# Kernel tuning notes

Measured on AMD Instinct MI355X. Metric: run time of the kernel, lower is better.

The kernel has to match this reference:

```python
import jax, jax.numpy as jnp
import numpy as np

N = 50000          # num nodes
E_RAND = 600000    # random edges (self-loops appended -> E = E_RAND + N)
HEADS = 4
OUT_CH = 16
OUT_NEURONS = 2 * OUT_CH   # diag reparam: [mean | std-logit]
IN_CH = 128
NEG_SLOPE = 0.2


def setup_inputs() -> dict:
    key = jax.random.key(0)
    k1, k2, k3, k4, k5 = jax.random.split(key, 5)
    x = jax.random.normal(k1, (N, IN_CH), jnp.float32)
    src = jax.random.randint(k2, (E_RAND,), 0, N, jnp.int32)
    dst = jax.random.randint(k3, (E_RAND,), 0, N, jnp.int32)
    loops = jnp.arange(N, dtype=jnp.int32)
    edge_index = jnp.stack([jnp.concatenate([src, loops]),
                            jnp.concatenate([dst, loops])])  # [2, E]
    # glorot init for weight [IN_CH, HEADS*OUT_NEURONS]
    s_w = float(np.sqrt(6.0 / (IN_CH + HEADS * OUT_NEURONS)))
    weight = jax.random.uniform(k4, (IN_CH, HEADS * OUT_NEURONS), jnp.float32, -s_w, s_w)
    # glorot for att [1, HEADS, 2*OUT_NEURONS]
    s_a = float(np.sqrt(6.0 / (HEADS + 2 * OUT_NEURONS)))
    att = jax.random.uniform(k5, (1, HEADS, 2 * OUT_NEURONS), jnp.float32, -s_a, s_a)
    bias = jnp.zeros((HEADS * OUT_NEURONS,), jnp.float32)
    return {"x": x, "edge_index": edge_index, "weight": weight, "att": att, "bias": bias}


def reference(x, edge_index, weight, att, bias):
    src, dst = edge_index[0], edge_index[1]  # j -> i (PyG source_to_target)
    h = (x @ weight).reshape(N, HEADS, OUT_NEURONS)          # Theta x
    x_j = h[src]                                             # [E, H, On]
    x_i = h[dst]                                             # [E, H, On]
    # alpha = LeakyReLU(a^T [x_i || x_j])
    alpha = (x_i * att[:, :, :OUT_NEURONS]).sum(-1) + \
            (x_j * att[:, :, OUT_NEURONS:]).sum(-1)          # [E, H]
    alpha = jax.nn.leaky_relu(alpha, NEG_SLOPE)
    # segment softmax over neighborhoods of target node i
    m = jax.ops.segment_max(alpha, dst, num_segments=N)      # [N, H]
    e = jnp.exp(alpha - m[dst])
    denom = jax.ops.segment_sum(e, dst, num_segments=N)      # [N, H]
    alpha = e / (denom[dst] + 1e-16)                          # [E, H]
    # scatter-add aggregation of attention-weighted features
    agg = jax.ops.segment_sum(x_j * alpha[:, :, None], dst, num_segments=N)  # [N, H, On]
    out = agg.reshape(N, HEADS * OUT_NEURONS) + bias
    # VIB diag reparameterization + closed-form KL against N(0, I)
    o = out.reshape(N * HEADS, OUT_NEURONS)
    mean = o[:, :OUT_CH]
    std = jax.nn.softplus(o[:, OUT_CH:] - 5.0) + 1e-10
    kl = (-jnp.log(std) + 0.5 * (std * std + mean * mean) - 0.5).sum(-1)  # [N*H]
    ixz = kl.reshape(N, HEADS).mean(-1)                      # [N]
    # eval + val_use_mean=True: output is the mean part
    out_final = mean.reshape(N, HEADS * OUT_CH)
    structure_kl_loss = jnp.zeros((), jnp.float32)
    return out_final, ixz, structure_kl_loss, mean, std
```

## Files before the change

kernel.cpp:

```cpp
#include <hip/hip_runtime.h>
#include <stdint.h>

#define NN 50000
#define NB 196
#define NTILES 782
#define NEG_SLOPE 0.2f
#define WTS 136

#define IXZ_OFF    (NN * 64)
#define SKL_OFF    (NN * 64 + NN)
#define MEAN_OFF   (NN * 64 + NN + 1)
#define STD_OFF    (MEAN_OFF + NN * 64)

typedef unsigned int u32;
typedef unsigned short u16;
typedef unsigned char u8;
typedef __attribute__((ext_vector_type(8))) short short8;
typedef __attribute__((ext_vector_type(4))) float f32x4;
typedef __attribute__((ext_vector_type(2))) float f32x2;

__device__ __forceinline__ float bf2f(u16 s) { return __uint_as_float(((u32)s) << 16); }
__device__ __forceinline__ u16 f2bf(float f) {
    u32 u = __float_as_uint(f);
    u += 0x7FFFu + ((u >> 16) & 1u);
    return (u16)(u >> 16);
}
__device__ __forceinline__ float lo16(u32 u) { return __uint_as_float(u << 16); }
__device__ __forceinline__ float hi16(u32 u) { return __uint_as_float(u & 0xFFFF0000u); }
__device__ __forceinline__ float softplusf(float x) {
    return fmaxf(x, 0.f) + log1pf(expf(-fabsf(x)));
}
__device__ __forceinline__ void stout(void* o, long long idx, float v, bool f32) {
    if (f32) ((float*)o)[idx] = v;
    else     ((u16*)o)[idx]   = f2bf(v);
}
__device__ __forceinline__ int wscan_incl(int v, int lane) {
#pragma unroll
    for (int off = 1; off < 64; off <<= 1) {
        int u = __shfl_up(v, off);
        if (lane >= off) v += u;
    }
    return v;
}

__device__ __forceinline__ bool detect_f32_block(const u32* __restrict__ xw,
                                                 int* lflag)
{
    const int t = threadIdx.x;
    if (t < 64) {
        u32 wrd = xw[t];
        u32 e = (wrd >> 7) & 0xFF;
        bool plaus = (e >= 0x60 && e <= 0x85);
        unsigned long long b = __ballot(plaus);
        if (t == 0) *lflag = (__popcll(b) < 32) ? 1 : 0;
    }
    __syncthreads();
    return *lflag != 0;
}

__global__ __launch_bounds__(256) void k_wt(const void* __restrict__ xv,
                                            const void* __restrict__ wv_,
                                            u16* __restrict__ wtg,
                                            int* __restrict__ zbase)
{
    __shared__ int lflag;
    const bool f32 = detect_f32_block((const u32*)xv, &lflag);
    const int t = threadIdx.x;

    for (int i = blockIdx.x * 256 + t; i < 2 * NN + 1; i += 64 * 256)
        zbase[i] = 0;

    if (blockIdx.x < 8) {
        const int k = blockIdx.x * 16 + (t >> 4);
        const int cq = t & 15;
        u16 v[8];
        if (f32) {
            const float* w = (const float*)wv_;
            float4 a = *(const float4*)(w + k * 128 + cq * 8);
            float4 b = *(const float4*)(w + k * 128 + cq * 8 + 4);
            v[0] = f2bf(a.x); v[1] = f2bf(a.y); v[2] = f2bf(a.z); v[3] = f2bf(a.w);
            v[4] = f2bf(b.x); v[5] = f2bf(b.y); v[6] = f2bf(b.z); v[7] = f2bf(b.w);
        } else {
            const u16* w = (const u16*)wv_;
            uint4 u = *(const uint4*)(w + k * 128 + cq * 8);
            v[0] = (u16)(u.x & 0xFFFF); v[1] = (u16)(u.x >> 16);
            v[2] = (u16)(u.y & 0xFFFF); v[3] = (u16)(u.y >> 16);
            v[4] = (u16)(u.z & 0xFFFF); v[5] = (u16)(u.z >> 16);
            v[6] = (u16)(u.w & 0xFFFF); v[7] = (u16)(u.w >> 16);
        }
#pragma unroll
        for (int j = 0; j < 8; j++)
            wtg[(cq * 8 + j) * WTS + k] = v[j];
    }
}

__global__ __launch_bounds__(256) void k_gemm(
    const void* __restrict__ xv, const u16* __restrict__ wtg,
    const void* __restrict__ attv, u8* __restrict__ hb,
    float* __restrict__ ai, float* __restrict__ aj,
    const int* __restrict__ dst, int* __restrict__ counts, int E)
{
    __shared__ __align__(16) u16 ls[128 * WTS];
    __shared__ int lflag;
    const bool f32 = detect_f32_block((const u32*)xv, &lflag);
    const int tid = threadIdx.x;

    {
        uint4* d = (uint4*)ls;
        const uint4* s = (const uint4*)wtg;
        for (int i = tid; i < 128 * WTS / 8; i += 256) d[i] = s[i];
    }

    const int w = tid >> 6, L = tid & 63;
    const int q = L >> 4, c15 = L & 15;
    const int nb16 = blockIdx.x * 64 + w * 16;

    short8 afr[4];
    {
        int nrow = nb16 + c15; if (nrow > NN - 1) nrow = NN - 1;
        if (f32) {
            const float* xp = (const float*)xv + (size_t)nrow * 128 + q * 8;
#pragma unroll
            for (int ks = 0; ks < 4; ks++) {
                float4 a = *(const float4*)(xp + ks * 32);
                float4 b = *(const float4*)(xp + ks * 32 + 4);
                union { short8 s; u16 e[8]; } u;
                u.e[0] = f2bf(a.x); u.e[1] = f2bf(a.y); u.e[2] = f2bf(a.z); u.e[3] = f2bf(a.w);
                u.e[4] = f2bf(b.x); u.e[5] = f2bf(b.y); u.e[6] = f2bf(b.z); u.e[7] = f2bf(b.w);
                afr[ks] = u.s;
            }
        } else {
            const u16* xp = (const u16*)xv + (size_t)nrow * 128 + q * 8;
#pragma unroll
            for (int ks = 0; ks < 4; ks++)
                afr[ks] = *(const short8*)(xp + ks * 32);
        }
    }
    __syncthreads();

    f32x4 acc[8];
#pragma unroll
    for (int t = 0; t < 8; t++) {
        acc[t] = (f32x4){0.f, 0.f, 0.f, 0.f};
        const u16* bp = ls + (16 * t + c15) * WTS + q * 8;
#pragma unroll
        for (int ks = 0; ks < 4; ks++) {
            short8 bfr = *(const short8*)(bp + ks * 32);
            acc[t] = __builtin_amdgcn_mfma_f32_16x16x32_bf16(afr[ks], bfr, acc[t], 0, 0, 0);
        }
    }

    float ati[8], atj[8];
#pragma unroll
    for (int t = 0; t < 8; t++) {
        int p = (t >> 1) * 64 + (t & 1) * 16 + c15;
        if (f32) {
            ati[t] = ((const float*)attv)[p];
            atj[t] = ((const float*)attv)[p + 32];
        } else {
            ati[t] = bf2f(((const u16*)attv)[p]);
            atj[t] = bf2f(((const u16*)attv)[p + 32]);
        }
    }
#pragma unroll
    for (int r = 0; r < 4; r++) {
        int node = nb16 + q * 4 + r;
#pragma unroll
        for (int h = 0; h < 4; h++) {
            float pi = acc[2 * h][r] * ati[2 * h] + acc[2 * h + 1][r] * ati[2 * h + 1];
            float pj = acc[2 * h][r] * atj[2 * h] + acc[2 * h + 1][r] * atj[2 * h + 1];
            pi += __shfl_xor(pi, 1); pj += __shfl_xor(pj, 1);
            pi += __shfl_xor(pi, 2); pj += __shfl_xor(pj, 2);
            pi += __shfl_xor(pi, 4); pj += __shfl_xor(pj, 4);
            pi += __shfl_xor(pi, 8); pj += __shfl_xor(pj, 8);
            if (c15 == 0 && node < NN) { ai[node * 4 + h] = pi; aj[node * 4 + h] = pj; }
        }
    }

    __syncthreads();
    u16* myls = ls + w * 16 * WTS;
#pragma unroll
    for (int t = 0; t < 8; t++)
#pragma unroll
        for (int r = 0; r < 4; r++)
            myls[(q * 4 + r) * WTS + 16 * t + c15] = f2bf(acc[t][r]);
#pragma unroll
    for (int v = 0; v < 4; v++) {
        int idx = v * 64 + L;
        int nrow = idx >> 4, c8 = idx & 15;
        int node = nb16 + nrow;
        uint4 t16 = *(const uint4*)(myls + nrow * WTS + c8 * 8);
        float f0 = lo16(t16.x), f1 = hi16(t16.x);
        float f2 = lo16(t16.y), f3 = hi16(t16.y);
        float f4 = lo16(t16.z), f5 = hi16(t16.z);
        float f6 = lo16(t16.w), f7 = hi16(t16.w);
        u32 lo = 0, hi = 0;
        lo = __builtin_amdgcn_cvt_pk_fp8_f32(f0, f1, lo, false);
        lo = __builtin_amdgcn_cvt_pk_fp8_f32(f2, f3, lo, true);
        hi = __builtin_amdgcn_cvt_pk_fp8_f32(f4, f5, hi, false);
        hi = __builtin_amdgcn_cvt_pk_fp8_f32(f6, f7, hi, true);
        if (node < NN) {
            uint2 o; o.x = lo; o.y = hi;
            *(uint2*)(hb + (size_t)node * 128 + c8 * 8) = o;
        }
    }

    const int gid = blockIdx.x * 256 + tid;
    const int stride = gridDim.x * 256;
    for (int e = gid; e < E; e += stride)
        atomicAdd(&counts[dst[e]], 1);
}

__global__ __launch_bounds__(256) void k_scan1(const int* __restrict__ counts,
                                               int* __restrict__ lexcl,
                                               int* __restrict__ blocksum,
                                               int* __restrict__ done,
                                               int* __restrict__ sboff_g)
{
    __shared__ int wsum[4];
    __shared__ int sboff[256];
    __shared__ int lastf;
    const int t = threadIdx.x, lane = t & 63, wv = t >> 6;
    const int i = blockIdx.x * 256 + t;
    int c = (i < NN) ? counts[i] : 0;
    int inc = wscan_incl(c, lane);
    if (lane == 63) wsum[wv] = inc;
    __syncthreads();
    int add = 0;
#pragma unroll
    for (int k = 0; k < 3; k++) if (k < wv) add += wsum[k];
    inc += add;
    if (i < NN) lexcl[i] = inc - c;
    if (t == 255) {
        blocksum[blockIdx.x] = inc;
        __threadfence();
        lastf = (atomicAdd(done, 1) == NB - 1) ? 1 : 0;
    }
    __syncthreads();
    if (lastf) {
        __threadfence();
        int c2 = (t < NB) ? blocksum[t] : 0;
        int inc2 = wscan_incl(c2, lane);
        if (lane == 63) wsum[wv] = inc2;
        __syncthreads();
        int add2 = 0;
#pragma unroll
        for (int k = 0; k < 3; k++) if (k < wv) add2 += wsum[k];
        sboff[t] = inc2 + add2 - c2;
        __syncthreads();
        sboff_g[t] = sboff[t];
    }
}

__global__ __launch_bounds__(256) void k_fill(
    const int* __restrict__ ei, const int* __restrict__ lexcl,
    const int* __restrict__ sboff_g, int* __restrict__ cursor,
    int* __restrict__ perm_src, int E)
{
    int e = blockIdx.x * 256 + threadIdx.x;
    if (e >= E) return;
    int d = ei[E + e];
    int pos = sboff_g[d >> 8] + lexcl[d] + atomicAdd(&cursor[d], 1);
    perm_src[pos] = ei[e];
}

__global__ __launch_bounds__(256) void k_agg(
    const int* __restrict__ lexcl, const int* __restrict__ sboff_g,
    const int* __restrict__ counts, const int* __restrict__ perm_src,
    const float* __restrict__ ai, const float* __restrict__ aj,
    const u8* __restrict__ hb, const void* __restrict__ biasv,
    const void* __restrict__ xv, void* __restrict__ outv)
{
    __shared__ int lflag;
    const bool f32 = detect_f32_block((const u32*)xv, &lflag);
    const int t = blockIdx.x * 256 + threadIdx.x;
    const int node = t >> 4;
    const int l = t & 15;
    const int head = l >> 2;
    const int cc0 = (l & 3) << 3;

    const int rs = sboff_g[node >> 8] + lexcl[node];
    const int re = rs + counts[node];
    const float ain = ai[node * 4 + head];
    const u8* hl8 = hb + l * 8;

    float dsum = 0.f;
    float a0 = 0.f, a1 = 0.f, a2 = 0.f, a3 = 0.f;
    float a4 = 0.f, a5 = 0.f, a6 = 0.f, a7 = 0.f;

    int i = rs;
    for (; i + 1 < re; i += 2) {
        int s0 = perm_src[i], s1 = perm_src[i + 1];
        float x0 = aj[s0 * 4 + head] + ain;
        float x1 = aj[s1 * 4 + head] + ain;
        x0 = x0 > 0.f ? x0 : NEG_SLOPE * x0;
        x1 = x1 > 0.f ? x1 : NEG_SLOPE * x1;
        float e0 = __expf(x0), e1 = __expf(x1);
        uint2 h0 = *(const uint2*)(hl8 + (size_t)s0 * 128);
        uint2 h1 = *(const uint2*)(hl8 + (size_t)s1 * 128);
        f32x2 p0 = __builtin_amdgcn_cvt_pk_f32_fp8(h0.x, false);
        f32x2 p1 = __builtin_amdgcn_cvt_pk_f32_fp8(h0.x, true);
        f32x2 p2 = __builtin_amdgcn_cvt_pk_f32_fp8(h0.y, false);
        f32x2 p3 = __builtin_amdgcn_cvt_pk_f32_fp8(h0.y, true);
        f32x2 q0 = __builtin_amdgcn_cvt_pk_f32_fp8(h1.x, false);
        f32x2 q1 = __builtin_amdgcn_cvt_pk_f32_fp8(h1.x, true);
        f32x2 q2 = __builtin_amdgcn_cvt_pk_f32_fp8(h1.y, false);
        f32x2 q3 = __builtin_amdgcn_cvt_pk_f32_fp8(h1.y, true);
        dsum += e0 + e1;
        a0 += e0 * p0.x + e1 * q0.x;  a1 += e0 * p0.y + e1 * q0.y;
        a2 += e0 * p1.x + e1 * q1.x;  a3 += e0 * p1.y + e1 * q1.y;
        a4 += e0 * p2.x + e1 * q2.x;  a5 += e0 * p2.y + e1 * q2.y;
        a6 += e0 * p3.x + e1 * q3.x;  a7 += e0 * p3.y + e1 * q3.y;
    }
    if (i < re) {
        int s0 = perm_src[i];
        float x0 = aj[s0 * 4 + head] + ain;
        x0 = x0 > 0.f ? x0 : NEG_SLOPE * x0;
        float e0 = __expf(x0);
        uint2 h0 = *(const uint2*)(hl8 + (size_t)s0 * 128);
        f32x2 p0 = __builtin_amdgcn_cvt_pk_f32_fp8(h0.x, false);
        f32x2 p1 = __builtin_amdgcn_cvt_pk_f32_fp8(h0.x, true);
        f32x2 p2 = __builtin_amdgcn_cvt_pk_f32_fp8(h0.y, false);
        f32x2 p3 = __builtin_amdgcn_cvt_pk_f32_fp8(h0.y, true);
        dsum += e0;
        a0 += e0 * p0.x; a1 += e0 * p0.y;
        a2 += e0 * p1.x; a3 += e0 * p1.y;
        a4 += e0 * p2.x; a5 += e0 * p2.y;
        a6 += e0 * p3.x; a7 += e0 * p3.y;
    }

    const float inv = 1.f / (dsum + 1e-16f);
    const int cb = head * 32 + cc0;
    float v[8];
    if (f32) {
        const float* bias = (const float*)biasv;
#pragma unroll
        for (int j = 0; j < 8; j++) v[j] = bias[cb + j];
    } else {
        const u16* bias = (const u16*)biasv;
#pragma unroll
        for (int j = 0; j < 8; j++) v[j] = bf2f(bias[cb + j]);
    }
    v[0] += a0 * inv; v[1] += a1 * inv; v[2] += a2 * inv; v[3] += a3 * inv;
    v[4] += a4 * inv; v[5] += a5 * inv; v[6] += a6 * inv; v[7] += a7 * inv;

    float part = 0.f;
    if (cc0 < 16) {
#pragma unroll
        for (int j = 0; j < 8; j++) part += 0.5f * v[j] * v[j];
        long long o = (long long)node * 64 + head * 16 + cc0;
#pragma unroll
        for (int j = 0; j < 8; j++) stout(outv, o + j, v[j], f32);
        long long om = (long long)MEAN_OFF + o;
#pragma unroll
        for (int j = 0; j < 8; j++) stout(outv, om + j, v[j], f32);
    } else {
        long long os = (long long)STD_OFF + (long long)node * 64 + head * 16 + (cc0 - 16);
#pragma unroll
        for (int j = 0; j < 8; j++) {
            float s = softplusf(v[j] - 5.f) + 1e-10f;
            part += -logf(s) + 0.5f * s * s - 0.5f;
            stout(outv, os + j, s, f32);
        }
    }
    part += __shfl_xor(part, 1); part += __shfl_xor(part, 2);
    part += __shfl_xor(part, 4); part += __shfl_xor(part, 8);
    if (l == 0) stout(outv, (long long)IXZ_OFF + node, part * 0.25f, f32);
    if (t == 0) stout(outv, (long long)SKL_OFF, 0.f, f32);
}

extern "C" void kernel_launch(void* const* d_in, const int* in_sizes, int n_in,
                              void* d_out, int out_size, void* d_ws, size_t ws_size,
                              hipStream_t stream)
{
    const void* x    = d_in[0];
    const int*  ei   = (const int*)d_in[1];
    const void* w    = d_in[2];
    const void* att  = d_in[3];
    const void* bias = d_in[4];
    int E = in_sizes[1] / 2;

    u8*    hb       = (u8*)d_ws;
    float* ai       = (float*)(hb + (size_t)NN * 128);
    float* aj       = ai + NN * 4;
    int*   perm_src = (int*)(aj + NN * 4);
    int*   counts   = perm_src + E;
    int*   cursor   = counts + NN;
    int*   done     = cursor + NN;
    int*   lexcl    = done + 1;
    int*   blocksum = lexcl + NN;
    int*   sboff_g  = blocksum + NB;
    u16*   wtg      = (u16*)(((uintptr_t)(sboff_g + 256) + 15) & ~(uintptr_t)15);

    k_wt<<<64, 256, 0, stream>>>(x, w, wtg, counts);
    k_gemm<<<NTILES, 256, 0, stream>>>(x, wtg, att, hb, ai, aj,
                                       ei + E, counts, E);
    k_scan1<<<NB, 256, 0, stream>>>(counts, lexcl, blocksum, done, sboff_g);
    k_fill<<<(E + 255) / 256, 256, 0, stream>>>(ei, lexcl, sboff_g,
                                                cursor, perm_src, E);
    k_agg<<<(NN * 16) / 256, 256, 0, stream>>>(lexcl, sboff_g, counts,
                                               perm_src, ai, aj, hb,
                                               bias, x, d_out);
}
```

Baseline: 208.2 us.

## Split edge counting into its own kernel, read GEMM weights from global, prefetch indices

The dst-count atomics move out of the GEMM into a separate k_cnt kernel. The GEMM stops staging the whole transposed weight in LDS and reads B fragments straight from global/L2, using only small per-wave LDS regions for the fp8 repack, which cuts LDS use per block and removes two barriers. The aggregation loop software-prefetches the next pair of source indices and aj logits so the gathers overlap the current iteration's work. A redundant LDS round-trip in the scan's block-offset write is also dropped. These trade an extra kernel launch and repeated global weight reads for higher occupancy and better latency hiding.

```diff
diff --git a/kernel.cpp b/kernel.cpp
--- a/kernel.cpp
+++ b/kernel.cpp
@@ -94,22 +94,22 @@
     }
 }
 
+__global__ __launch_bounds__(256) void k_cnt(const int* __restrict__ dst,
+                                             int* __restrict__ counts, int E)
+{
+    int e = blockIdx.x * 256 + threadIdx.x;
+    if (e < E) atomicAdd(&counts[dst[e]], 1);
+}
+
 __global__ __launch_bounds__(256) void k_gemm(
     const void* __restrict__ xv, const u16* __restrict__ wtg,
     const void* __restrict__ attv, u8* __restrict__ hb,
-    float* __restrict__ ai, float* __restrict__ aj,
-    const int* __restrict__ dst, int* __restrict__ counts, int E)
-{
-    __shared__ __align__(16) u16 ls[128 * WTS];
+    float* __restrict__ ai, float* __restrict__ aj)
+{
+    __shared__ __align__(16) u16 rp[4][16 * WTS];
     __shared__ int lflag;
     const bool f32 = detect_f32_block((const u32*)xv, &lflag);
     const int tid = threadIdx.x;
-
-    {
-        uint4* d = (uint4*)ls;
-        const uint4* s = (const uint4*)wtg;
-        for (int i = tid; i < 128 * WTS / 8; i += 256) d[i] = s[i];
-    }
 
     const int w = tid >> 6, L = tid & 63;
     const int q = L >> 4, c15 = L & 15;
@@ -136,13 +136,12 @@
                 afr[ks] = *(const short8*)(xp + ks * 32);
         }
     }
-    __syncthreads();
 
     f32x4 acc[8];
 #pragma unroll
     for (int t = 0; t < 8; t++) {
         acc[t] = (f32x4){0.f, 0.f, 0.f, 0.f};
-        const u16* bp = ls + (16 * t + c15) * WTS + q * 8;
+        const u16* bp = wtg + (16 * t + c15) * WTS + q * 8;
 #pragma unroll
         for (int ks = 0; ks < 4; ks++) {
             short8 bfr = *(const short8*)(bp + ks * 32);
@@ -177,8 +176,7 @@
         }
     }
 
-    __syncthreads();
-    u16* myls = ls + w * 16 * WTS;
+    u16* myls = rp[w];
 #pragma unroll
     for (int t = 0; t < 8; t++)
 #pragma unroll
@@ -204,11 +202,6 @@
             *(uint2*)(hb + (size_t)node * 128 + c8 * 8) = o;
         }
     }
-
-    const int gid = blockIdx.x * 256 + tid;
-    const int stride = gridDim.x * 256;
-    for (int e = gid; e < E; e += stride)
-        atomicAdd(&counts[dst[e]], 1);
 }
 
 __global__ __launch_bounds__(256) void k_scan1(const int* __restrict__ counts,
@@ -218,7 +211,6 @@
                                                int* __restrict__ sboff_g)
 {
     __shared__ int wsum[4];
-    __shared__ int sboff[256];
     __shared__ int lastf;
     const int t = threadIdx.x, lane = t & 63, wv = t >> 6;
     const int i = blockIdx.x * 256 + t;
@@ -246,9 +238,7 @@
         int add2 = 0;
 #pragma unroll
         for (int k = 0; k < 3; k++) if (k < wv) add2 += wsum[k];
-        sboff[t] = inc2 + add2 - c2;
-        __syncthreads();
-        sboff_g[t] = sboff[t];
+        sboff_g[t] = inc2 + add2 - c2;
     }
 }
 
@@ -289,15 +279,21 @@
     float a4 = 0.f, a5 = 0.f, a6 = 0.f, a7 = 0.f;
 
     int i = rs;
-    for (; i + 1 < re; i += 2) {
-        int s0 = perm_src[i], s1 = perm_src[i + 1];
-        float x0 = aj[s0 * 4 + head] + ain;
-        float x1 = aj[s1 * 4 + head] + ain;
-        x0 = x0 > 0.f ? x0 : NEG_SLOPE * x0;
-        x1 = x1 > 0.f ? x1 : NEG_SLOPE * x1;
+    int sA = 0, sB = 0;
+    float ajA = 0.f, ajB = 0.f;
+    if (i < re)     { sA = perm_src[i];     ajA = aj[sA * 4 + head]; }
+    if (i + 1 < re) { sB = perm_src[i + 1]; ajB = aj[sB * 4 + head]; }
+
+    while (i + 1 < re) {
+        uint2 h0 = *(const uint2*)(hl8 + (size_t)sA * 128);
+        uint2 h1 = *(const uint2*)(hl8 + (size_t)sB * 128);
+        int i2 = i + 2;
+        int sC = 0, sD = 0; float ajC = 0.f, ajD = 0.f;
+        if (i2 < re)     { sC = perm_src[i2];     ajC = aj[sC * 4 + head]; }
+        if (i2 + 1 < re) { sD = perm_src[i2 + 1]; ajD = aj[sD * 4 + head]; }
+        float x0 = ajA + ain; x0 = x0 > 0.f ? x0 : NEG_SLOPE * x0;
+        float x1 = ajB + ain; x1 = x1 > 0.f ? x1 : NEG_SLOPE * x1;
         float e0 = __expf(x0), e1 = __expf(x1);
-        uint2 h0 = *(const uint2*)(hl8 + (size_t)s0 * 128);
-        uint2 h1 = *(const uint2*)(hl8 + (size_t)s1 * 128);
         f32x2 p0 = __builtin_amdgcn_cvt_pk_f32_fp8(h0.x, false);
         f32x2 p1 = __builtin_amdgcn_cvt_pk_f32_fp8(h0.x, true);
         f32x2 p2 = __builtin_amdgcn_cvt_pk_f32_fp8(h0.y, false);
@@ -311,13 +307,12 @@
         a2 += e0 * p1.x + e1 * q1.x;  a3 += e0 * p1.y + e1 * q1.y;
         a4 += e0 * p2.x + e1 * q2.x;  a5 += e0 * p2.y + e1 * q2.y;
         a6 += e0 * p3.x + e1 * q3.x;  a7 += e0 * p3.y + e1 * q3.y;
+        i = i2; sA = sC; sB = sD; ajA = ajC; ajB = ajD;
     }
     if (i < re) {
-        int s0 = perm_src[i];
-        float x0 = aj[s0 * 4 + head] + ain;
-        x0 = x0 > 0.f ? x0 : NEG_SLOPE * x0;
+        uint2 h0 = *(const uint2*)(hl8 + (size_t)sA * 128);
+        float x0 = ajA + ain; x0 = x0 > 0.f ? x0 : NEG_SLOPE * x0;
         float e0 = __expf(x0);
-        uint2 h0 = *(const uint2*)(hl8 + (size_t)s0 * 128);
         f32x2 p0 = __builtin_amdgcn_cvt_pk_f32_fp8(h0.x, false);
         f32x2 p1 = __builtin_amdgcn_cvt_pk_f32_fp8(h0.x, true);
         f32x2 p2 = __builtin_amdgcn_cvt_pk_f32_fp8(h0.y, false);
@@ -393,8 +388,8 @@
     u16*   wtg      = (u16*)(((uintptr_t)(sboff_g + 256) + 15) & ~(uintptr_t)15);
 
     k_wt<<<64, 256, 0, stream>>>(x, w, wtg, counts);
-    k_gemm<<<NTILES, 256, 0, stream>>>(x, wtg, att, hb, ai, aj,
-                                       ei + E, counts, E);
+    k_cnt<<<(E + 255) / 256, 256, 0, stream>>>(ei + E, counts, E);
+    k_gemm<<<NTILES, 256, 0, stream>>>(x, wtg, att, hb, ai, aj);
     k_scan1<<<NB, 256, 0, stream>>>(counts, lexcl, blocksum, done, sboff_g);
     k_fill<<<(E + 255) / 256, 256, 0, stream>>>(ei, lexcl, sboff_g,
                                                 cursor, perm_src, E);
```

New measurement: 219.8 us. +5.6%, slower.
